# Kernel tuning notes

Measured on AMD Instinct MI355X. Metric: run time of the kernel, lower is better.

Reference implementation:

```python
import jax, jax.numpy as jnp
import numpy as np
from jax import lax

V, D, H, L, K = 50257, 1024, 2048, 6, 3
B, S = 4, 2048
EPS = 1.1920929e-07  # torch.finfo(float32).eps (torch RMSNorm default eps=None)


def rmsnorm(x, w):
    return x * lax.rsqrt(jnp.mean(x * x, axis=-1, keepdims=True) + EPS) * w


def depthwise_conv(x, w, b):
    # x: (B,S,D), w: (D,1,K) depthwise kernel, padding='same' as in torch Conv1d
    y = lax.conv_general_dilated(x.transpose(0, 2, 1), w, (1,), 'SAME',
                                 dimension_numbers=('NCH', 'OIH', 'NCH'),
                                 feature_group_count=x.shape[-1])
    return y.transpose(0, 2, 1) + b


def mingru(x, h0, wz, bz, wh, bh, wo, bo):
    # minGRU: z=sigmoid(Wz x), h_tilde=Wh x, h_t=(1-z_t)h_{t-1}+z_t h_tilde_t (parallel scan)
    z = jax.nn.sigmoid(jnp.einsum('bsd,hd->bsh', x, wz) + bz)
    htil = jnp.einsum('bsd,hd->bsh', x, wh) + bh
    a, bc = 1.0 - z, z * htil

    def comb(c1, c2):
        a1, b1 = c1
        a2, b2 = c2
        return a1 * a2, a2 * b1 + b2

    A, Bc = lax.associative_scan(comb, (a, bc), axis=1)
    h = A * h0[:, None, :] + Bc                      # (B,S,H)
    out = jnp.einsum('bsh,dh->bsd', h, wo) + bo      # project back to model dim
    return out, h[:, -1]


def setup_inputs():
    key = jax.random.key(0)
    ks = jax.random.split(key, 16)
    sc = 0.02
    p = {}
    p['x'] = jax.random.randint(ks[0], (B, S), 0, V)
    p['h_prev'] = jax.random.normal(ks[1], (B, L, H), jnp.float32)
    p['emb'] = jax.random.normal(ks[2], (V, D), jnp.float32) * sc
    p['conv_dw_w'] = jax.random.normal(ks[3], (L, D, 1, K), jnp.float32) * sc
    p['conv_dw_b'] = jnp.zeros((L, D), jnp.float32)
    p['conv_pw_w'] = jax.random.normal(ks[4], (L, D, D), jnp.float32) * sc
    p['conv_pw_b'] = jnp.zeros((L, D), jnp.float32)
    p['n1_w'] = jnp.ones((L, D), jnp.float32)
    p['wz'] = jax.random.normal(ks[5], (L, H, D), jnp.float32) * sc
    p['bz'] = jnp.zeros((L, H), jnp.float32)
    p['wh'] = jax.random.normal(ks[6], (L, H, D), jnp.float32) * sc
    p['bh'] = jnp.zeros((L, H), jnp.float32)
    p['wo'] = jax.random.normal(ks[7], (L, D, H), jnp.float32) * sc
    p['bo'] = jnp.zeros((L, D), jnp.float32)
    p['n2_w'] = jnp.ones((L, D), jnp.float32)
    p['f1_w'] = jax.random.normal(ks[8], (L, H, D), jnp.float32) * sc
    p['f1_b'] = jnp.zeros((L, H), jnp.float32)
    p['f2_w'] = jax.random.normal(ks[9], (L, D, H), jnp.float32) * sc
    p['f2_b'] = jnp.zeros((L, D), jnp.float32)
    p['norm_w'] = jnp.ones((D,), jnp.float32)
    p['out_w'] = jax.random.normal(ks[10], (H, D), jnp.float32) * sc
    p['out_b'] = jnp.zeros((H,), jnp.float32)
    return p


def reference(x, h_prev, emb, conv_dw_w, conv_dw_b, conv_pw_w, conv_pw_b, n1_w,
              wz, bz, wh, bh, wo, bo, n2_w, f1_w, f1_b, f2_w, f2_b,
              norm_w, out_w, out_b):
    xe = emb[x]                                      # (B,S,D)
    h_next = []
    for l in range(L):
        c = depthwise_conv(xe, conv_dw_w[l], conv_dw_b[l])
        c = jnp.einsum('bsd,ed->bse', c, conv_pw_w[l]) + conv_pw_b[l]  # 1x1 conv
        xe = c + xe
        g, hl = mingru(rmsnorm(xe, n1_w[l]), h_prev[:, l],
                       wz[l], bz[l], wh[l], bh[l], wo[l], bo[l])
        xe = g + xe
        f = rmsnorm(xe, n2_w[l])
        f = jnp.einsum('bsd,hd->bsh', f, f1_w[l]) + f1_b[l]
        f = jax.nn.gelu(f, approximate=False)
        f = jnp.einsum('bsh,dh->bsd', f, f2_w[l]) + f2_b[l]
        xe = f + xe
        h_next.append(hl)
    out = jnp.einsum('bsd,hd->bsh', rmsnorm(xe, norm_w), out_w) + out_b
    return out, jnp.stack(h_next, axis=1)             # (B,S,H), (B,L,H)
```

## Files before the change

kernel.cpp:

```cpp
#include <hip/hip_runtime.h>

typedef __bf16 bf16x8 __attribute__((ext_vector_type(8)));
typedef float f32x4 __attribute__((ext_vector_type(4)));

#define DEVI __device__ __forceinline__

namespace {
constexpr int cB = 4, cS = 2048, cD = 1024, cH = 2048, cL = 6;
constexpr int cM = cB * cS;
constexpr float cEPS = 1.1920929e-07f;
constexpr int NCH = 16, CHS = cS / NCH;
}

DEVI unsigned short f2bf(float f) {
  union { float f; unsigned u; } c; c.f = f;
  const unsigned u = c.u;
  return (unsigned short)((u + 0x7fffu + ((u >> 16) & 1u)) >> 16);
}
DEVI float bf2f(unsigned short h) {
  union { unsigned u; float f; } c; c.u = ((unsigned)h) << 16;
  return c.f;
}

DEVI void gld16(const void* g, void* l) {
  __builtin_amdgcn_global_load_lds(
      (__attribute__((address_space(1))) void*)g,
      (__attribute__((address_space(3))) void*)l, 16, 0, 0);
}

union F4 { float4 v; float a[4]; };

__global__ __launch_bounds__(256) void embed_k(const int* __restrict__ x,
    const float* __restrict__ emb, float* __restrict__ xe) {
  const int bs = blockIdx.x;
  const int idx = x[bs];
  const int t = threadIdx.x;
  *(float4*)&xe[(size_t)bs * cD + t * 4] =
      *(const float4*)&emb[(size_t)idx * cD + t * 4];
}

__global__ __launch_bounds__(256) void dwconv_k(const float* __restrict__ xe,
    const float* __restrict__ w, const float* __restrict__ bias,
    unsigned short* __restrict__ out) {
  const int bs = blockIdx.x;
  const int s = bs & (cS - 1);
  const int t = threadIdx.x;
  const int d = t * 4;
  const size_t base = (size_t)bs * cD + d;
  F4 x0, xm, xp, vb;
  x0.v = *(const float4*)&xe[base];
  xm.v = make_float4(0.f, 0.f, 0.f, 0.f);
  xp.v = make_float4(0.f, 0.f, 0.f, 0.f);
  if (s > 0) xm.v = *(const float4*)&xe[base - cD];
  if (s < cS - 1) xp.v = *(const float4*)&xe[base + cD];
  vb.v = *(const float4*)&bias[d];
  unsigned short o[4];
#pragma unroll
  for (int j = 0; j < 4; ++j) {
    const float w0 = w[(d + j) * 3 + 0];
    const float w1 = w[(d + j) * 3 + 1];
    const float w2 = w[(d + j) * 3 + 2];
    o[j] = f2bf(xm.a[j] * w0 + x0.a[j] * w1 + xp.a[j] * w2 + vb.a[j]);
  }
  *(ushort4*)&out[base] = make_ushort4(o[0], o[1], o[2], o[3]);
}

__global__ __launch_bounds__(256) void rmsnorm_k(const float* __restrict__ x,
    const float* __restrict__ w, unsigned short* __restrict__ o) {
  const int row = blockIdx.x;
  const int t = threadIdx.x;
  const size_t base = (size_t)row * cD + t * 4;
  F4 v; v.v = *(const float4*)&x[base];
  float ss = v.a[0]*v.a[0] + v.a[1]*v.a[1] + v.a[2]*v.a[2] + v.a[3]*v.a[3];
#pragma unroll
  for (int off = 32; off > 0; off >>= 1) ss += __shfl_down(ss, off, 64);
  __shared__ float red[4];
  if ((t & 63) == 0) red[t >> 6] = ss;
  __syncthreads();
  const float scale = rsqrtf((red[0]+red[1]+red[2]+red[3]) * (1.f/cD) + cEPS);
  F4 wv; wv.v = *(const float4*)&w[t * 4];
  *(ushort4*)&o[base] = make_ushort4(
      f2bf(v.a[0]*scale*wv.a[0]), f2bf(v.a[1]*scale*wv.a[1]),
      f2bf(v.a[2]*scale*wv.a[2]), f2bf(v.a[3]*scale*wv.a[3]));
}

__global__ __launch_bounds__(256) void cvt_k(const float* __restrict__ s,
    unsigned short* __restrict__ d, int n) {
  const int i = (blockIdx.x * 256 + threadIdx.x) * 4;
  if (i >= n) return;
  F4 v; v.v = *(const float4*)&s[i];
  *(ushort4*)&d[i] = make_ushort4(f2bf(v.a[0]), f2bf(v.a[1]),
                                  f2bf(v.a[2]), f2bf(v.a[3]));
}

template<int N, int K, int EPI>
__global__ __launch_bounds__(256) void gemm_bt(
    const unsigned short* __restrict__ A, const unsigned short* __restrict__ W,
    const float* __restrict__ bias, float* __restrict__ Cf,
    unsigned short* __restrict__ Cb) {
  __shared__ unsigned short As[128 * 32];
  __shared__ unsigned short Bs[128 * 32];
  const int t = threadIdx.x;
  const int lane = t & 63;
  const int wave = t >> 6;
  const int m0 = blockIdx.x * 128;
  const int n0 = blockIdx.y * 128;
  const int wm = (wave >> 1) * 64;
  const int wn = (wave & 1) * 64;
  const int fr = lane & 15;
  const int fk = (lane >> 4) * 8;

  const int arow = t >> 2;
  const int acol = (t & 3) * 8;
  const unsigned short* gA = A + (size_t)(m0 + arow) * K + acol;
  const unsigned short* gB = W + (size_t)(n0 + arow) * K + acol;
  unsigned short* lA = As + wave * 512;
  unsigned short* lB = Bs + wave * 512;

  f32x4 acc[4][4] = {};
  for (int k0 = 0; k0 < K; k0 += 32) {
    gld16(gA + k0, lA);
    gld16(gA + k0 + (size_t)64 * K, lA + 2048);
    gld16(gB + k0, lB);
    gld16(gB + k0 + (size_t)64 * K, lB + 2048);
    __syncthreads();
    bf16x8 fa[4], fb[4];
#pragma unroll
    for (int i = 0; i < 4; ++i) {
      fa[i] = *(const bf16x8*)&As[(wm + i * 16 + fr) * 32 + fk];
      fb[i] = *(const bf16x8*)&Bs[(wn + i * 16 + fr) * 32 + fk];
    }
#pragma unroll
    for (int i = 0; i < 4; ++i)
#pragma unroll
      for (int j = 0; j < 4; ++j)
        acc[i][j] = __builtin_amdgcn_mfma_f32_16x16x32_bf16(
            fa[i], fb[j], acc[i][j], 0, 0, 0);
    __syncthreads();
  }

  const int r0 = m0 + wm + ((lane >> 4) << 2);
  const int c0 = n0 + wn + fr;
#pragma unroll
  for (int i = 0; i < 4; ++i)
#pragma unroll
    for (int j = 0; j < 4; ++j) {
      const int col = c0 + j * 16;
      const float bv = bias[col];
#pragma unroll
      for (int r = 0; r < 4; ++r) {
        const size_t idx = (size_t)(r0 + i * 16 + r) * N + col;
        const float v = acc[i][j][r] + bv;
        if constexpr (EPI == 0) {
          Cf[idx] = v;
        } else if constexpr (EPI == 1) {
          Cf[idx] += v;
        } else if constexpr (EPI == 2) {
          Cb[idx] = f2bf(1.f / (1.f + __expf(-v)));
        } else if constexpr (EPI == 3) {
          Cb[idx] = f2bf(v);
        } else {
          Cb[idx] = f2bf(0.5f * v * (1.f + erff(v * 0.70710678118654752f)));
        }
      }
    }
}

__global__ __launch_bounds__(256) void scan1_k(const unsigned short* __restrict__ z,
    const unsigned short* __restrict__ ht, float* __restrict__ Ac,
    float* __restrict__ Bc) {
  const int tid = blockIdx.x * 256 + threadIdx.x;
  const int hp = (tid & (cH / 2 - 1)) * 2;
  const int ck = (tid / (cH / 2)) & (NCH - 1);
  const int b = tid / ((cH / 2) * NCH);
  const size_t base = ((size_t)b * cS + (size_t)ck * CHS) * cH + hp;
  float a0 = 1.f, s0 = 0.f, a1 = 1.f, s1 = 0.f;
#pragma unroll 4
  for (int s = 0; s < CHS; ++s) {
    const unsigned zz = *(const unsigned*)&z[base + (size_t)s * cH];
    const unsigned hh = *(const unsigned*)&ht[base + (size_t)s * cH];
    const float z0 = bf2f((unsigned short)(zz & 0xffff)), z1 = bf2f((unsigned short)(zz >> 16));
    const float t0 = bf2f((unsigned short)(hh & 0xffff)), t1 = bf2f((unsigned short)(hh >> 16));
    const float aa0 = 1.f - z0, aa1 = 1.f - z1;
    s0 = aa0 * s0 + z0 * t0; a0 *= aa0;
    s1 = aa1 * s1 + z1 * t1; a1 *= aa1;
  }
  const size_t so = ((size_t)b * NCH + ck) * cH + hp;
  *(float2*)&Ac[so] = make_float2(a0, a1);
  *(float2*)&Bc[so] = make_float2(s0, s1);
}

__global__ __launch_bounds__(256) void scan2_k(const float* __restrict__ Ac,
    const float* __restrict__ Bc, const float* __restrict__ h_prev,
    float* __restrict__ P, float* __restrict__ hn, int l) {
  const int tid = blockIdx.x * 256 + threadIdx.x;
  const int h = tid & (cH - 1);
  const int b = tid >> 11;
  float run = h_prev[((size_t)b * cL + l) * cH + h];
#pragma unroll
  for (int c = 0; c < NCH; ++c) {
    const size_t so = ((size_t)b * NCH + c) * cH + h;
    P[so] = run;
    run = Ac[so] * run + Bc[so];
  }
  hn[((size_t)b * cL + l) * cH + h] = run;
}

__global__ __launch_bounds__(256) void scan3_k(const unsigned short* __restrict__ z,
    unsigned short* __restrict__ ht, const float* __restrict__ P) {
  const int tid = blockIdx.x * 256 + threadIdx.x;
  const int hp = (tid & (cH / 2 - 1)) * 2;
  const int ck = (tid / (cH / 2)) & (NCH - 1);
  const int b = tid / ((cH / 2) * NCH);
  const size_t base = ((size_t)b * cS + (size_t)ck * CHS) * cH + hp;
  const size_t so = ((size_t)b * NCH + ck) * cH + hp;
  const float2 rr = *(const float2*)&P[so];
  float r0 = rr.x, r1 = rr.y;
#pragma unroll 4
  for (int s = 0; s < CHS; ++s) {
    const unsigned zz = *(const unsigned*)&z[base + (size_t)s * cH];
    const unsigned hh = *(const unsigned*)&ht[base + (size_t)s * cH];
    const float z0 = bf2f((unsigned short)(zz & 0xffff)), z1 = bf2f((unsigned short)(zz >> 16));
    const float t0 = bf2f((unsigned short)(hh & 0xffff)), t1 = bf2f((unsigned short)(hh >> 16));
    r0 = (1.f - z0) * r0 + z0 * t0;
    r1 = (1.f - z1) * r1 + z1 * t1;
    *(unsigned*)&ht[base + (size_t)s * cH] =
        (unsigned)f2bf(r0) | ((unsigned)f2bf(r1) << 16);
  }
}

extern "C" void kernel_launch(void* const* d_in, const int* in_sizes, int n_in,
                              void* d_out, int out_size, void* d_ws, size_t ws_size,
                              hipStream_t stream) {
  (void)in_sizes; (void)n_in; (void)out_size; (void)ws_size;
  const int*   x      = (const int*)d_in[0];
  const float* h_prev = (const float*)d_in[1];
  const float* emb    = (const float*)d_in[2];
  const float* cdw_w  = (const float*)d_in[3];
  const float* cdw_b  = (const float*)d_in[4];
  const float* cpw_w  = (const float*)d_in[5];
  const float* cpw_b  = (const float*)d_in[6];
  const float* n1w    = (const float*)d_in[7];
  const float* wzp    = (const float*)d_in[8];
  const float* bzp    = (const float*)d_in[9];
  const float* whp    = (const float*)d_in[10];
  const float* bhp    = (const float*)d_in[11];
  const float* wop    = (const float*)d_in[12];
  const float* bop    = (const float*)d_in[13];
  const float* n2w    = (const float*)d_in[14];
  const float* f1wp   = (const float*)d_in[15];
  const float* f1bp   = (const float*)d_in[16];
  const float* f2wp   = (const float*)d_in[17];
  const float* f2bp   = (const float*)d_in[18];
  const float* nw     = (const float*)d_in[19];
  const float* owp    = (const float*)d_in[20];
  const float* obp    = (const float*)d_in[21];

  float* out_main = (float*)d_out;
  float* out_hn   = out_main + (size_t)cM * cH;

  char* p = (char*)d_ws;
  auto alloc = [&](size_t bytes) {
    char* r = p; p += (bytes + 255) & ~(size_t)255; return r;
  };
  float*          xe = (float*)alloc((size_t)cM * cD * 4);
  unsigned short* xn = (unsigned short*)alloc((size_t)cM * cD * 2);
  unsigned short* zb = (unsigned short*)alloc((size_t)cM * cH * 2);
  unsigned short* hb = (unsigned short*)alloc((size_t)cM * cH * 2);
  float* Ac = (float*)alloc((size_t)cB * NCH * cH * 4);
  float* Bc = (float*)alloc((size_t)cB * NCH * cH * 4);
  float* Pr = (float*)alloc((size_t)cB * NCH * cH * 4);
  unsigned short* w_pw = (unsigned short*)alloc((size_t)cD * cD * 2);
  unsigned short* w_z  = (unsigned short*)alloc((size_t)cH * cD * 2);
  unsigned short* w_h  = (unsigned short*)alloc((size_t)cH * cD * 2);
  unsigned short* w_o  = (unsigned short*)alloc((size_t)cD * cH * 2);
  unsigned short* w_f1 = (unsigned short*)alloc((size_t)cH * cD * 2);
  unsigned short* w_f2 = (unsigned short*)alloc((size_t)cD * cH * 2);

  auto cvt = [&](const float* src, unsigned short* dst, size_t n) {
    cvt_k<<<dim3((unsigned)(n / 1024)), 256, 0, stream>>>(src, dst, (int)n);
  };

  embed_k<<<cM, 256, 0, stream>>>(x, emb, xe);

  for (int l = 0; l < cL; ++l) {
    cvt(cpw_w + (size_t)l * cD * cD, w_pw, (size_t)cD * cD);
    cvt(wzp  + (size_t)l * cH * cD, w_z,  (size_t)cH * cD);
    cvt(whp  + (size_t)l * cH * cD, w_h,  (size_t)cH * cD);
    cvt(wop  + (size_t)l * cD * cH, w_o,  (size_t)cD * cH);
    cvt(f1wp + (size_t)l * cH * cD, w_f1, (size_t)cH * cD);
    cvt(f2wp + (size_t)l * cD * cH, w_f2, (size_t)cD * cH);

    dwconv_k<<<cM, 256, 0, stream>>>(xe, cdw_w + (size_t)l * cD * 3,
                                     cdw_b + (size_t)l * cD, xn);
    gemm_bt<cD, cD, 1><<<dim3(cM / 128, cD / 128), 256, 0, stream>>>(
        xn, w_pw, cpw_b + (size_t)l * cD, xe, nullptr);

    rmsnorm_k<<<cM, 256, 0, stream>>>(xe, n1w + (size_t)l * cD, xn);
    gemm_bt<cH, cD, 2><<<dim3(cM / 128, cH / 128), 256, 0, stream>>>(
        xn, w_z, bzp + (size_t)l * cH, nullptr, zb);
    gemm_bt<cH, cD, 3><<<dim3(cM / 128, cH / 128), 256, 0, stream>>>(
        xn, w_h, bhp + (size_t)l * cH, nullptr, hb);
    scan1_k<<<cB * NCH * (cH / 2) / 256, 256, 0, stream>>>(zb, hb, Ac, Bc);
    scan2_k<<<cB * cH / 256, 256, 0, stream>>>(Ac, Bc, h_prev, Pr, out_hn, l);
    scan3_k<<<cB * NCH * (cH / 2) / 256, 256, 0, stream>>>(zb, hb, Pr);
    gemm_bt<cD, cH, 1><<<dim3(cM / 128, cD / 128), 256, 0, stream>>>(
        hb, w_o, bop + (size_t)l * cD, xe, nullptr);

    rmsnorm_k<<<cM, 256, 0, stream>>>(xe, n2w + (size_t)l * cD, xn);
    gemm_bt<cH, cD, 4><<<dim3(cM / 128, cH / 128), 256, 0, stream>>>(
        xn, w_f1, f1bp + (size_t)l * cH, nullptr, zb);
    gemm_bt<cD, cH, 1><<<dim3(cM / 128, cD / 128), 256, 0, stream>>>(
        zb, w_f2, f2bp + (size_t)l * cD, xe, nullptr);
  }

  rmsnorm_k<<<cM, 256, 0, stream>>>(xe, nw, xn);
  cvt(owp, w_z, (size_t)cH * cD);
  gemm_bt<cH, cD, 0><<<dim3(cM / 128, cH / 128), 256, 0, stream>>>(
      xn, w_z, obp, out_main, nullptr);
}
```

Before: 2.397 ms.

## Fuse z/h GEMMs, merge scan passes, swizzle tiles, batch weight conversion

The z and h projections now run as one GEMM with a doubled N that routes each tile to the right weight, bias and output buffer. The scan2 and scan3 kernels are merged so each chunk recomputes its carry prefix itself. The GEMM also gets a workgroup-ID swizzle for better L2 reuse and a bf16 epilogue staged through LDS for coalesced 16-byte stores. Weight conversion to bf16 is hoisted out of the layer loop into one batched pass per tensor, at the cost of more workspace and a larger shared-memory footprint.

```diff
diff --git a/kernel.cpp b/kernel.cpp
--- a/kernel.cpp
+++ b/kernel.cpp
@@ -93,18 +93,35 @@
                                   f2bf(v.a[2]), f2bf(v.a[3]));
 }
 
-template<int N, int K, int EPI>
+template<int N, int K, int EPI, int NS>
 __global__ __launch_bounds__(256) void gemm_bt(
-    const unsigned short* __restrict__ A, const unsigned short* __restrict__ W,
-    const float* __restrict__ bias, float* __restrict__ Cf,
-    unsigned short* __restrict__ Cb) {
-  __shared__ unsigned short As[128 * 32];
-  __shared__ unsigned short Bs[128 * 32];
+    const unsigned short* __restrict__ A,
+    const unsigned short* __restrict__ W0,
+    const unsigned short* __restrict__ W1,
+    const float* __restrict__ bias0, const float* __restrict__ bias1,
+    float* __restrict__ Cf, unsigned short* __restrict__ Cb,
+    unsigned short* __restrict__ Cb2) {
+  __shared__ unsigned short lds[128 * 136];
+  unsigned short* As = lds;
+  unsigned short* Bs = lds + 4096;
   const int t = threadIdx.x;
   const int lane = t & 63;
   const int wave = t >> 6;
-  const int m0 = blockIdx.x * 128;
-  const int n0 = blockIdx.y * 128;
+
+  constexpr int GX = 64;
+  constexpr unsigned nwg = GX * (N / 128);
+  const unsigned id = blockIdx.y * GX + blockIdx.x;
+  const unsigned sw = (id & 7u) * (nwg >> 3) + (id >> 3);
+  const int m0 = (int)(sw & (GX - 1)) * 128;
+  const int n0 = (int)(sw >> 6) * 128;
+
+  const bool zpart = (n0 < NS);
+  const unsigned short* Wp = zpart ? W0 : W1;
+  const int nw0 = zpart ? n0 : n0 - NS;
+  const float* bp = zpart ? bias0 : bias1;
+  constexpr int CW0 = NS, CW1 = N - NS;
+  const int CW = zpart ? CW0 : (CW1 > 0 ? CW1 : 1);
+
   const int wm = (wave >> 1) * 64;
   const int wn = (wave & 1) * 64;
   const int fr = lane & 15;
@@ -113,7 +130,7 @@
   const int arow = t >> 2;
   const int acol = (t & 3) * 8;
   const unsigned short* gA = A + (size_t)(m0 + arow) * K + acol;
-  const unsigned short* gB = W + (size_t)(n0 + arow) * K + acol;
+  const unsigned short* gB = Wp + (size_t)(nw0 + arow) * K + acol;
   unsigned short* lA = As + wave * 512;
   unsigned short* lB = Bs + wave * 512;
 
@@ -139,31 +156,54 @@
     __syncthreads();
   }
 
-  const int r0 = m0 + wm + ((lane >> 4) << 2);
-  const int c0 = n0 + wn + fr;
-#pragma unroll
-  for (int i = 0; i < 4; ++i)
-#pragma unroll
-    for (int j = 0; j < 4; ++j) {
-      const int col = c0 + j * 16;
-      const float bv = bias[col];
-#pragma unroll
-      for (int r = 0; r < 4; ++r) {
-        const size_t idx = (size_t)(r0 + i * 16 + r) * N + col;
-        const float v = acc[i][j][r] + bv;
-        if constexpr (EPI == 0) {
-          Cf[idx] = v;
-        } else if constexpr (EPI == 1) {
-          Cf[idx] += v;
-        } else if constexpr (EPI == 2) {
-          Cb[idx] = f2bf(1.f / (1.f + __expf(-v)));
-        } else if constexpr (EPI == 3) {
-          Cb[idx] = f2bf(v);
-        } else {
-          Cb[idx] = f2bf(0.5f * v * (1.f + erff(v * 0.70710678118654752f)));
+  const int r0l = wm + ((lane >> 4) << 2);
+  const int c0l = wn + fr;
+
+  if constexpr (EPI <= 1) {
+#pragma unroll
+    for (int i = 0; i < 4; ++i)
+#pragma unroll
+      for (int j = 0; j < 4; ++j) {
+        const int col = nw0 + c0l + j * 16;
+        const float bv = bp[col];
+#pragma unroll
+        for (int r = 0; r < 4; ++r) {
+          const size_t idx = (size_t)(m0 + r0l + i * 16 + r) * CW + col;
+          const float v = acc[i][j][r] + bv;
+          if constexpr (EPI == 1) Cf[idx] += v;
+          else                    Cf[idx] = v;
         }
       }
+  } else {
+    unsigned short* cb = zpart ? Cb : Cb2;
+#pragma unroll
+    for (int i = 0; i < 4; ++i)
+#pragma unroll
+      for (int j = 0; j < 4; ++j) {
+        const int col = c0l + j * 16;
+        const float bv = bp[nw0 + col];
+#pragma unroll
+        for (int r = 0; r < 4; ++r) {
+          const float v = acc[i][j][r] + bv;
+          unsigned short o;
+          if constexpr (EPI == 4) {
+            o = f2bf(0.5f * v * (1.f + erff(v * 0.70710678118654752f)));
+          } else {
+            o = zpart ? f2bf(1.f / (1.f + __expf(-v))) : f2bf(v);
+          }
+          lds[(r0l + i * 16 + r) * 136 + col] = o;
+        }
+      }
+    __syncthreads();
+#pragma unroll
+    for (int it = 0; it < 8; ++it) {
+      const int flat = it * 256 + t;
+      const int row = flat >> 4;
+      const int ch = flat & 15;
+      const float4 v = *(const float4*)&lds[row * 136 + ch * 8];
+      *(float4*)&cb[(size_t)(m0 + row) * CW + nw0 + ch * 8] = v;
     }
+  }
 }
 
 __global__ __launch_bounds__(256) void scan1_k(const unsigned short* __restrict__ z,
@@ -190,32 +230,25 @@
   *(float2*)&Bc[so] = make_float2(s0, s1);
 }
 
-__global__ __launch_bounds__(256) void scan2_k(const float* __restrict__ Ac,
+__global__ __launch_bounds__(256) void scan23_k(const unsigned short* __restrict__ z,
+    unsigned short* __restrict__ ht, const float* __restrict__ Ac,
     const float* __restrict__ Bc, const float* __restrict__ h_prev,
-    float* __restrict__ P, float* __restrict__ hn, int l) {
-  const int tid = blockIdx.x * 256 + threadIdx.x;
-  const int h = tid & (cH - 1);
-  const int b = tid >> 11;
-  float run = h_prev[((size_t)b * cL + l) * cH + h];
-#pragma unroll
-  for (int c = 0; c < NCH; ++c) {
-    const size_t so = ((size_t)b * NCH + c) * cH + h;
-    P[so] = run;
-    run = Ac[so] * run + Bc[so];
-  }
-  hn[((size_t)b * cL + l) * cH + h] = run;
-}
-
-__global__ __launch_bounds__(256) void scan3_k(const unsigned short* __restrict__ z,
-    unsigned short* __restrict__ ht, const float* __restrict__ P) {
+    float* __restrict__ hn, int l) {
   const int tid = blockIdx.x * 256 + threadIdx.x;
   const int hp = (tid & (cH / 2 - 1)) * 2;
   const int ck = (tid / (cH / 2)) & (NCH - 1);
   const int b = tid / ((cH / 2) * NCH);
+  const size_t hoff = ((size_t)b * cL + l) * cH + hp;
+  const float2 h0 = *(const float2*)&h_prev[hoff];
+  float r0 = h0.x, r1 = h0.y;
+  for (int c = 0; c < ck; ++c) {
+    const size_t so = ((size_t)b * NCH + c) * cH + hp;
+    const float2 av = *(const float2*)&Ac[so];
+    const float2 bv = *(const float2*)&Bc[so];
+    r0 = av.x * r0 + bv.x;
+    r1 = av.y * r1 + bv.y;
+  }
   const size_t base = ((size_t)b * cS + (size_t)ck * CHS) * cH + hp;
-  const size_t so = ((size_t)b * NCH + ck) * cH + hp;
-  const float2 rr = *(const float2*)&P[so];
-  float r0 = rr.x, r1 = rr.y;
 #pragma unroll 4
   for (int s = 0; s < CHS; ++s) {
     const unsigned zz = *(const unsigned*)&z[base + (size_t)s * cH];
@@ -227,6 +260,7 @@
     *(unsigned*)&ht[base + (size_t)s * cH] =
         (unsigned)f2bf(r0) | ((unsigned)f2bf(r1) << 16);
   }
+  if (ck == NCH - 1) *(float2*)&hn[hoff] = make_float2(r0, r1);
 }
 
 extern "C" void kernel_launch(void* const* d_in, const int* in_sizes, int n_in,
@@ -269,53 +303,58 @@
   unsigned short* hb = (unsigned short*)alloc((size_t)cM * cH * 2);
   float* Ac = (float*)alloc((size_t)cB * NCH * cH * 4);
   float* Bc = (float*)alloc((size_t)cB * NCH * cH * 4);
-  float* Pr = (float*)alloc((size_t)cB * NCH * cH * 4);
-  unsigned short* w_pw = (unsigned short*)alloc((size_t)cD * cD * 2);
-  unsigned short* w_z  = (unsigned short*)alloc((size_t)cH * cD * 2);
-  unsigned short* w_h  = (unsigned short*)alloc((size_t)cH * cD * 2);
-  unsigned short* w_o  = (unsigned short*)alloc((size_t)cD * cH * 2);
-  unsigned short* w_f1 = (unsigned short*)alloc((size_t)cH * cD * 2);
-  unsigned short* w_f2 = (unsigned short*)alloc((size_t)cD * cH * 2);
+  unsigned short* w_pw = (unsigned short*)alloc((size_t)cL * cD * cD * 2);
+  unsigned short* w_z  = (unsigned short*)alloc((size_t)cL * cH * cD * 2);
+  unsigned short* w_h  = (unsigned short*)alloc((size_t)cL * cH * cD * 2);
+  unsigned short* w_o  = (unsigned short*)alloc((size_t)cL * cD * cH * 2);
+  unsigned short* w_f1 = (unsigned short*)alloc((size_t)cL * cH * cD * 2);
+  unsigned short* w_f2 = (unsigned short*)alloc((size_t)cL * cD * cH * 2);
+  unsigned short* w_ow = (unsigned short*)alloc((size_t)cH * cD * 2);
 
   auto cvt = [&](const float* src, unsigned short* dst, size_t n) {
     cvt_k<<<dim3((unsigned)(n / 1024)), 256, 0, stream>>>(src, dst, (int)n);
   };
 
+  cvt(cpw_w, w_pw, (size_t)cL * cD * cD);
+  cvt(wzp,  w_z,  (size_t)cL * cH * cD);
+  cvt(whp,  w_h,  (size_t)cL * cH * cD);
+  cvt(wop,  w_o,  (size_t)cL * cD * cH);
+  cvt(f1wp, w_f1, (size_t)cL * cH * cD);
+  cvt(f2wp, w_f2, (size_t)cL * cD * cH);
+  cvt(owp,  w_ow, (size_t)cH * cD);
+
   embed_k<<<cM, 256, 0, stream>>>(x, emb, xe);
 
   for (int l = 0; l < cL; ++l) {
-    cvt(cpw_w + (size_t)l * cD * cD, w_pw, (size_t)cD * cD);
-    cvt(wzp  + (size_t)l * cH * cD, w_z,  (size_t)cH * cD);
-    cvt(whp  + (size_t)l * cH * cD, w_h,  (size_t)cH * cD);
-    cvt(wop  + (size_t)l * cD * cH, w_o,  (size_t)cD * cH);
-    cvt(f1wp + (size_t)l * cH * cD, w_f1, (size_t)cH * cD);
-    cvt(f2wp + (size_t)l * cD * cH, w_f2, (size_t)cD * cH);
+    const size_t oDD = (size_t)l * cD * cD, oHD = (size_t)l * cH * cD;
 
     dwconv_k<<<cM, 256, 0, stream>>>(xe, cdw_w + (size_t)l * cD * 3,
                                      cdw_b + (size_t)l * cD, xn);
-    gemm_bt<cD, cD, 1><<<dim3(cM / 128, cD / 128), 256, 0, stream>>>(
-        xn, w_pw, cpw_b + (size_t)l * cD, xe, nullptr);
+    gemm_bt<cD, cD, 1, cD><<<dim3(64, cD / 128), 256, 0, stream>>>(
+        xn, w_pw + oDD, w_pw + oDD, cpw_b + (size_t)l * cD,
+        cpw_b + (size_t)l * cD, xe, nullptr, nullptr);
 
     rmsnorm_k<<<cM, 256, 0, stream>>>(xe, n1w + (size_t)l * cD, xn);
-    gemm_bt<cH, cD, 2><<<dim3(cM / 128, cH / 128), 256, 0, stream>>>(
-        xn, w_z, bzp + (size_t)l * cH, nullptr, zb);
-    gemm_bt<cH, cD, 3><<<dim3(cM / 128, cH / 128), 256, 0, stream>>>(
-        xn, w_h, bhp + (size_t)l * cH, nullptr, hb);
+    gemm_bt<2 * cH, cD, 5, cH><<<dim3(64, 2 * cH / 128), 256, 0, stream>>>(
+        xn, w_z + oHD, w_h + oHD, bzp + (size_t)l * cH, bhp + (size_t)l * cH,
+        nullptr, zb, hb);
     scan1_k<<<cB * NCH * (cH / 2) / 256, 256, 0, stream>>>(zb, hb, Ac, Bc);
-    scan2_k<<<cB * cH / 256, 256, 0, stream>>>(Ac, Bc, h_prev, Pr, out_hn, l);
-    scan3_k<<<cB * NCH * (cH / 2) / 256, 256, 0, stream>>>(zb, hb, Pr);
-    gemm_bt<cD, cH, 1><<<dim3(cM / 128, cD / 128), 256, 0, stream>>>(
-        hb, w_o, bop + (size_t)l * cD, xe, nullptr);
+    scan23_k<<<cB * NCH * (cH / 2) / 256, 256, 0, stream>>>(zb, hb, Ac, Bc,
+                                                            h_prev, out_hn, l);
+    gemm_bt<cD, cH, 1, cD><<<dim3(64, cD / 128), 256, 0, stream>>>(
+        hb, w_o + oHD, w_o + oHD, bop + (size_t)l * cD, bop + (size_t)l * cD,
+        xe, nullptr, nullptr);
 
     rmsnorm_k<<<cM, 256, 0, stream>>>(xe, n2w + (size_t)l * cD, xn);
-    gemm_bt<cH, cD, 4><<<dim3(cM / 128, cH / 128), 256, 0, stream>>>(
-        xn, w_f1, f1bp + (size_t)l * cH, nullptr, zb);
-    gemm_bt<cD, cH, 1><<<dim3(cM / 128, cD / 128), 256, 0, stream>>>(
-        zb, w_f2, f2bp + (size_t)l * cD, xe, nullptr);
+    gemm_bt<cH, cD, 4, cH><<<dim3(64, cH / 128), 256, 0, stream>>>(
+        xn, w_f1 + oHD, w_f1 + oHD, f1bp + (size_t)l * cH, f1bp + (size_t)l * cH,
+        nullptr, zb, nullptr);
+    gemm_bt<cD, cH, 1, cD><<<dim3(64, cD / 128), 256, 0, stream>>>(
+        zb, w_f2 + oHD, w_f2 + oHD, f2bp + (size_t)l * cD, f2bp + (size_t)l * cD,
+        xe, nullptr, nullptr);
   }
 
   rmsnorm_k<<<cM, 256, 0, stream>>>(xe, nw, xn);
-  cvt(owp, w_z, (size_t)cH * cD);
-  gemm_bt<cH, cD, 0><<<dim3(cM / 128, cH / 128), 256, 0, stream>>>(
-      xn, w_z, obp, out_main, nullptr);
-}
+  gemm_bt<cH, cD, 0, cH><<<dim3(64, cH / 128), 256, 0, stream>>>(
+      xn, w_ow, w_ow, obp, obp, out_main, nullptr, nullptr);
+}
```

After: 2.806 ms. +17.1%, slower.
